# Kernel optimization log

Hardware: AMD Instinct MI355X
Metric: run time of the kernel (lower is better)

The kernel has to match this reference:

```python
import jax, jax.numpy as jnp
import numpy as np

RECON_W = 0.1
CONT_W = 0.2
EPS = 1e-7  # BCE log clamp (torch clamps log at -100; eps-clip is the jax analogue)


def setup_inputs() -> dict:
    key = jax.random.key(0)
    k1, k2, k3, k4 = jax.random.split(key, 4)
    B, M = 256, 4096
    predictions = jax.random.uniform(k1, (B, M, 9), dtype=jnp.float32)
    targets = jax.random.uniform(k2, (B, M, 9), dtype=jnp.float32)
    reconstructed = jax.random.normal(k3, (B, 1, 128, 128), dtype=jnp.float32)
    images = jax.random.normal(k4, (B, 1, 128, 128), dtype=jnp.float32)
    return {"predictions": predictions, "targets": targets,
            "reconstructed": reconstructed, "images": images}


def _continuity_loss(p3, valid_mask):
    # p3: [B, M, 2]; valid_mask: [B, M] bool
    # For each valid slot i, find the next valid slot j > i and accumulate
    # mean(|p3[i] - p3[j]|) -- vectorized replacement for the ragged double loop.
    B, M, _ = p3.shape
    idx = jnp.arange(M, dtype=jnp.int32)
    BIG = jnp.int32(M)
    pos = jnp.where(valid_mask, idx[None, :], BIG)              # [B, M]
    # suffix min over j >= i of pos, then shift to get strict j > i
    suf = jnp.flip(jax.lax.cummin(jnp.flip(pos, axis=1), axis=1), axis=1)
    nxt = jnp.concatenate([suf[:, 1:], jnp.full((B, 1), BIG, jnp.int32)], axis=1)
    pair_valid = valid_mask & (nxt < BIG)                       # [B, M]
    nxt_c = jnp.clip(nxt, 0, M - 1)
    p3_next = jnp.take_along_axis(p3, nxt_c[..., None], axis=1)  # [B, M, 2]
    dist = jnp.abs(p3 - p3_next).mean(axis=-1)                  # [B, M]
    return jnp.sum(dist * pair_valid.astype(p3.dtype)) / B


def _loss(predictions, targets, reconstructed, images):
    target_curves = targets[..., :8]
    target_validity = targets[..., 8:9]
    valid_mask = target_validity[..., 0] > 0.5                  # [B, M]
    fmask = valid_mask.astype(predictions.dtype)
    n_valid = jnp.sum(fmask)

    def masked_l1(pred, tgt, width):
        num = jnp.sum(jnp.abs(pred - tgt) * fmask[..., None])
        return jnp.where(n_valid > 0, num / jnp.maximum(n_valid * width, 1.0), 0.0)

    coord_loss = masked_l1(predictions[..., :6], target_curves[..., :6], 6.0)
    width_loss = masked_l1(predictions[..., 6:8], target_curves[..., 6:8], 2.0)

    p = jnp.clip(predictions[..., 8:9], EPS, 1.0 - EPS)
    t = target_validity
    validity_loss = jnp.mean(-(t * jnp.log(p) + (1.0 - t) * jnp.log(1.0 - p)))

    continuity_loss = _continuity_loss(predictions[..., 4:6], valid_mask)
    reconstruction_loss = jnp.mean((reconstructed - images) ** 2)

    total = (coord_loss + width_loss + 2.0 * validity_loss
             + CONT_W * continuity_loss + RECON_W * reconstruction_loss)
    return total


def reference(predictions, targets, reconstructed, images):
    return _loss(predictions, targets, reconstructed, images)
```

## Files before the change

### kernel.cpp

```cpp
#include <hip/hip_runtime.h>
#include <math.h>

#define B_DIM 256
#define M_DIM 4096
#define EPSV 1e-7f


__global__ __launch_bounds__(1024) void main_loss_kernel(
    const float* __restrict__ pred, const float* __restrict__ tgt,
    double* __restrict__ ws)
{
    __shared__ float s_p4[M_DIM];
    __shared__ float s_p5[M_DIM];
    __shared__ unsigned long long s_words[M_DIM / 64];
    __shared__ float s_red[16][5];

    const int b    = blockIdx.x;
    const int t    = threadIdx.x;
    const int lane = t & 63;
    const int wave = t >> 6;

    const float* prow = pred + (size_t)b * M_DIM * 9;
    const float* trow = tgt  + (size_t)b * M_DIM * 9;

    float coord_s = 0.f, width_s = 0.f, val_s = 0.f, nval_s = 0.f;
    bool valid_k[4];

    #pragma unroll
    for (int k = 0; k < 4; ++k) {
        const int m = k * 1024 + t;
        const float* p = prow + m * 9;
        const float* q = trow + m * 9;
        float p0 = p[0], p1 = p[1], p2 = p[2], p3 = p[3], p4 = p[4],
              p5 = p[5], p6 = p[6], p7 = p[7], p8 = p[8];
        float t0 = q[0], t1 = q[1], t2 = q[2], t3 = q[3], t4 = q[4],
              t5 = q[5], t6 = q[6], t7 = q[7], t8 = q[8];

        bool valid = (t8 > 0.5f);
        float fm = valid ? 1.f : 0.f;
        coord_s += fm * (fabsf(p0 - t0) + fabsf(p1 - t1) + fabsf(p2 - t2) +
                         fabsf(p3 - t3) + fabsf(p4 - t4) + fabsf(p5 - t5));
        width_s += fm * (fabsf(p6 - t6) + fabsf(p7 - t7));
        nval_s  += fm;

        float pc = fminf(fmaxf(p8, EPSV), 1.0f - EPSV);
        val_s += -(t8 * logf(pc) + (1.0f - t8) * logf(1.0f - pc));

        s_p4[m] = p4;
        s_p5[m] = p5;
        valid_k[k] = valid;

        unsigned long long bal = __ballot(valid);
        if (lane == 0) s_words[k * 16 + wave] = bal;
    }
    __syncthreads();

    float cont_s = 0.f;
    #pragma unroll
    for (int k = 0; k < 4; ++k) {
        if (!valid_k[k]) continue;
        const int m   = k * 1024 + t;
        const int w   = m >> 6;
        const int bit = m & 63;
        unsigned long long mask = s_words[w];
        mask &= (bit == 63) ? 0ULL : (~0ULL << (bit + 1));
        int nxt = -1;
        if (mask) {
            nxt = (w << 6) + __builtin_ctzll(mask);
        } else {
            for (int w2 = w + 1; w2 < (M_DIM / 64); ++w2) {
                unsigned long long mw = s_words[w2];
                if (mw) { nxt = (w2 << 6) + __builtin_ctzll(mw); break; }
            }
        }
        if (nxt >= 0) {
            cont_s += 0.5f * (fabsf(s_p4[m] - s_p4[nxt]) +
                              fabsf(s_p5[m] - s_p5[nxt]));
        }
    }

    float vals[5] = {coord_s, width_s, val_s, nval_s, cont_s};
    #pragma unroll
    for (int i = 0; i < 5; ++i) {
        float v = vals[i];
        #pragma unroll
        for (int off = 32; off > 0; off >>= 1) v += __shfl_down(v, off, 64);
        vals[i] = v;
    }
    if (lane == 0) {
        #pragma unroll
        for (int i = 0; i < 5; ++i) s_red[wave][i] = vals[i];
    }
    __syncthreads();
    if (t == 0) {
        float acc[5] = {0.f, 0.f, 0.f, 0.f, 0.f};
        for (int wv = 0; wv < 16; ++wv)
            #pragma unroll
            for (int i = 0; i < 5; ++i) acc[i] += s_red[wv][i];
        atomicAdd(&ws[0], (double)acc[0]);
        atomicAdd(&ws[1], (double)acc[1]);
        atomicAdd(&ws[2], (double)acc[2]);
        atomicAdd(&ws[3], (double)acc[3]);
        atomicAdd(&ws[4], (double)acc[4]);
    }
}

__global__ __launch_bounds__(256) void recon_kernel(
    const float4* __restrict__ rec, const float4* __restrict__ img,
    double* __restrict__ ws, int n4)
{
    int idx    = blockIdx.x * blockDim.x + threadIdx.x;
    int stride = gridDim.x * blockDim.x;
    float s = 0.f;
    for (int i = idx; i < n4; i += stride) {
        float4 r  = rec[i];
        float4 im = img[i];
        float d0 = r.x - im.x, d1 = r.y - im.y, d2 = r.z - im.z, d3 = r.w - im.w;
        s += d0 * d0 + d1 * d1 + d2 * d2 + d3 * d3;
    }
    #pragma unroll
    for (int off = 32; off > 0; off >>= 1) s += __shfl_down(s, off, 64);
    __shared__ float sred[4];
    int lane = threadIdx.x & 63, wave = threadIdx.x >> 6;
    if (lane == 0) sred[wave] = s;
    __syncthreads();
    if (threadIdx.x == 0) {
        float a = sred[0] + sred[1] + sred[2] + sred[3];
        atomicAdd(&ws[5], (double)a);
    }
}

__global__ void finalize_kernel(const double* __restrict__ ws,
                                float* __restrict__ out)
{
    double coord_num = ws[0];
    double width_num = ws[1];
    double val_sum   = ws[2];
    double nv        = ws[3];
    double cont      = ws[4];
    double recon     = ws[5];

    double coord = (nv > 0.0) ? coord_num / fmax(nv * 6.0, 1.0) : 0.0;
    double width = (nv > 0.0) ? width_num / fmax(nv * 2.0, 1.0) : 0.0;
    double validity = val_sum / ((double)B_DIM * (double)M_DIM);
    double contl    = cont / (double)B_DIM;
    double reconl   = recon / ((double)B_DIM * 128.0 * 128.0);

    out[0] = (float)(coord + width + 2.0 * validity + 0.2 * contl + 0.1 * reconl);
}

extern "C" void kernel_launch(void* const* d_in, const int* in_sizes, int n_in,
                              void* d_out, int out_size, void* d_ws, size_t ws_size,
                              hipStream_t stream) {
    const float* pred = (const float*)d_in[0];
    const float* tgt  = (const float*)d_in[1];
    const float* rec  = (const float*)d_in[2];
    const float* img  = (const float*)d_in[3];
    double* ws = (double*)d_ws;

    hipMemsetAsync(d_ws, 0, 6 * sizeof(double), stream);

    main_loss_kernel<<<B_DIM, 1024, 0, stream>>>(pred, tgt, ws);

    const int n4 = (B_DIM * 128 * 128) / 4;
    recon_kernel<<<1024, 256, 0, stream>>>((const float4*)rec, (const float4*)img, ws, n4);

    finalize_kernel<<<1, 1, 0, stream>>>(ws, (float*)d_out);
}
```

Baseline: 156.2 us.

## Fuse loss, reconstruction and finalize into one kernel with coalesced float4 loads

Merges the main loss, reconstruction MSE and finalize kernels into a single launch. Extra blocks handle the MSE, and a last-block-done atomic counter computes the final scalar. The main path now reads prediction and target rows as coalesced float4 vectors instead of stride-9 scalar loads, taking validity bits from a ballot bitmask built in an earlier pass over column 8. It also switches to fast __logf. The cost is an extra strided read of column 8 and a per-element bitmask lookup, plus slightly lower log precision.

```diff
diff --git a/kernel.cpp b/kernel.cpp
--- a/kernel.cpp
+++ b/kernel.cpp
@@ -4,149 +4,170 @@
 #define B_DIM 256
 #define M_DIM 4096
 #define EPSV 1e-7f
+#define ROW_FLOATS (M_DIM * 9)
+#define ROW_F4     (ROW_FLOATS / 4)
+#define THREADS    1024
+#define RECON_BLOCKS 256
+#define GRID (B_DIM + RECON_BLOCKS)
 
 
-__global__ __launch_bounds__(1024) void main_loss_kernel(
+__global__ __launch_bounds__(1024) void fused_loss_kernel(
     const float* __restrict__ pred, const float* __restrict__ tgt,
-    double* __restrict__ ws)
+    const float4* __restrict__ rec, const float4* __restrict__ img,
+    double* __restrict__ ws, float* __restrict__ out)
 {
     __shared__ float s_p4[M_DIM];
     __shared__ float s_p5[M_DIM];
     __shared__ unsigned long long s_words[M_DIM / 64];
     __shared__ float s_red[16][5];
 
-    const int b    = blockIdx.x;
     const int t    = threadIdx.x;
     const int lane = t & 63;
     const int wave = t >> 6;
 
-    const float* prow = pred + (size_t)b * M_DIM * 9;
-    const float* trow = tgt  + (size_t)b * M_DIM * 9;
+    if (blockIdx.x >= B_DIM) {
+        const int n4     = (B_DIM * 128 * 128) / 4;
+        const int stride = RECON_BLOCKS * THREADS;
+        int idx = (blockIdx.x - B_DIM) * THREADS + t;
+        float s = 0.f;
+        #pragma unroll
+        for (int i = 0; i < 4; ++i) {
+            float4 r = rec[idx]; float4 m = img[idx];
+            float d0 = r.x - m.x, d1 = r.y - m.y, d2 = r.z - m.z, d3 = r.w - m.w;
+            s += d0 * d0 + d1 * d1 + d2 * d2 + d3 * d3;
+            idx += stride;
+        }
+        #pragma unroll
+        for (int off = 32; off > 0; off >>= 1) s += __shfl_down(s, off, 64);
+        if (lane == 0) s_red[wave][0] = s;
+        __syncthreads();
+        if (t == 0) {
+            float a = 0.f;
+            for (int w = 0; w < 16; ++w) a += s_red[w][0];
+            atomicAdd(&ws[5], (double)a);
+        }
+    } else {
+        const int b = blockIdx.x;
+        const float* prow = pred + (size_t)b * ROW_FLOATS;
+        const float* trow = tgt  + (size_t)b * ROW_FLOATS;
 
-    float coord_s = 0.f, width_s = 0.f, val_s = 0.f, nval_s = 0.f;
-    bool valid_k[4];
+        float val_s = 0.f, nval_s = 0.f;
+        bool valid_k[4];
+        #pragma unroll
+        for (int k = 0; k < 4; ++k) {
+            const int m = k * 1024 + t;
+            float t8 = trow[m * 9 + 8];
+            float p8 = prow[m * 9 + 8];
+            bool valid = (t8 > 0.5f);
+            valid_k[k] = valid;
+            nval_s += valid ? 1.f : 0.f;
+            float pc = fminf(fmaxf(p8, EPSV), 1.0f - EPSV);
+            val_s += -(t8 * __logf(pc) + (1.0f - t8) * __logf(1.0f - pc));
+            unsigned long long bal = __ballot(valid);
+            if (lane == 0) s_words[k * 16 + wave] = bal;
+        }
+        __syncthreads();
 
-    #pragma unroll
-    for (int k = 0; k < 4; ++k) {
-        const int m = k * 1024 + t;
-        const float* p = prow + m * 9;
-        const float* q = trow + m * 9;
-        float p0 = p[0], p1 = p[1], p2 = p[2], p3 = p[3], p4 = p[4],
-              p5 = p[5], p6 = p[6], p7 = p[7], p8 = p[8];
-        float t0 = q[0], t1 = q[1], t2 = q[2], t3 = q[3], t4 = q[4],
-              t5 = q[5], t6 = q[6], t7 = q[7], t8 = q[8];
-
-        bool valid = (t8 > 0.5f);
-        float fm = valid ? 1.f : 0.f;
-        coord_s += fm * (fabsf(p0 - t0) + fabsf(p1 - t1) + fabsf(p2 - t2) +
-                         fabsf(p3 - t3) + fabsf(p4 - t4) + fabsf(p5 - t5));
-        width_s += fm * (fabsf(p6 - t6) + fabsf(p7 - t7));
-        nval_s  += fm;
-
-        float pc = fminf(fmaxf(p8, EPSV), 1.0f - EPSV);
-        val_s += -(t8 * logf(pc) + (1.0f - t8) * logf(1.0f - pc));
-
-        s_p4[m] = p4;
-        s_p5[m] = p5;
-        valid_k[k] = valid;
-
-        unsigned long long bal = __ballot(valid);
-        if (lane == 0) s_words[k * 16 + wave] = bal;
-    }
-    __syncthreads();
-
-    float cont_s = 0.f;
-    #pragma unroll
-    for (int k = 0; k < 4; ++k) {
-        if (!valid_k[k]) continue;
-        const int m   = k * 1024 + t;
-        const int w   = m >> 6;
-        const int bit = m & 63;
-        unsigned long long mask = s_words[w];
-        mask &= (bit == 63) ? 0ULL : (~0ULL << (bit + 1));
-        int nxt = -1;
-        if (mask) {
-            nxt = (w << 6) + __builtin_ctzll(mask);
-        } else {
-            for (int w2 = w + 1; w2 < (M_DIM / 64); ++w2) {
-                unsigned long long mw = s_words[w2];
-                if (mw) { nxt = (w2 << 6) + __builtin_ctzll(mw); break; }
+        float coord_s = 0.f, width_s = 0.f;
+        const float4* pf4 = (const float4*)prow;
+        const float4* tf4 = (const float4*)trow;
+        #pragma unroll
+        for (int i = 0; i < ROW_F4 / THREADS; ++i) {
+            int f = i * THREADS + t;
+            float4 pv = pf4[f];
+            float4 tv = tf4[f];
+            int j0 = f * 4;
+            int m  = j0 / 9;
+            int c  = j0 - m * 9;
+            float pe[4] = {pv.x, pv.y, pv.z, pv.w};
+            float te[4] = {tv.x, tv.y, tv.z, tv.w};
+            #pragma unroll
+            for (int k = 0; k < 4; ++k) {
+                float fm = (float)((s_words[m >> 6] >> (m & 63)) & 1ULL);
+                float ad = fabsf(pe[k] - te[k]);
+                if (c < 6)      coord_s += fm * ad;
+                else if (c < 8) width_s += fm * ad;
+                if (c == 4)      s_p4[m] = pe[k];
+                else if (c == 5) s_p5[m] = pe[k];
+                ++c; if (c == 9) { c = 0; ++m; }
             }
         }
-        if (nxt >= 0) {
-            cont_s += 0.5f * (fabsf(s_p4[m] - s_p4[nxt]) +
-                              fabsf(s_p5[m] - s_p5[nxt]));
+        __syncthreads();
+
+        float cont_s = 0.f;
+        #pragma unroll
+        for (int k = 0; k < 4; ++k) {
+            if (!valid_k[k]) continue;
+            const int m   = k * 1024 + t;
+            const int w   = m >> 6;
+            const int bit = m & 63;
+            unsigned long long mask = s_words[w];
+            mask &= (bit == 63) ? 0ULL : (~0ULL << (bit + 1));
+            int nxt = -1;
+            if (mask) {
+                nxt = (w << 6) + __builtin_ctzll(mask);
+            } else {
+                for (int w2 = w + 1; w2 < (M_DIM / 64); ++w2) {
+                    unsigned long long mw = s_words[w2];
+                    if (mw) { nxt = (w2 << 6) + __builtin_ctzll(mw); break; }
+                }
+            }
+            if (nxt >= 0) {
+                cont_s += 0.5f * (fabsf(s_p4[m] - s_p4[nxt]) +
+                                  fabsf(s_p5[m] - s_p5[nxt]));
+            }
+        }
+
+        float vals[5] = {coord_s, width_s, val_s, nval_s, cont_s};
+        #pragma unroll
+        for (int i = 0; i < 5; ++i) {
+            float v = vals[i];
+            #pragma unroll
+            for (int off = 32; off > 0; off >>= 1) v += __shfl_down(v, off, 64);
+            vals[i] = v;
+        }
+        if (lane == 0) {
+            #pragma unroll
+            for (int i = 0; i < 5; ++i) s_red[wave][i] = vals[i];
+        }
+        __syncthreads();
+        if (t == 0) {
+            float acc[5] = {0.f, 0.f, 0.f, 0.f, 0.f};
+            for (int wv = 0; wv < 16; ++wv)
+                #pragma unroll
+                for (int i = 0; i < 5; ++i) acc[i] += s_red[wv][i];
+            atomicAdd(&ws[0], (double)acc[0]);
+            atomicAdd(&ws[1], (double)acc[1]);
+            atomicAdd(&ws[2], (double)acc[2]);
+            atomicAdd(&ws[3], (double)acc[3]);
+            atomicAdd(&ws[4], (double)acc[4]);
         }
     }
 
-    float vals[5] = {coord_s, width_s, val_s, nval_s, cont_s};
-    #pragma unroll
-    for (int i = 0; i < 5; ++i) {
-        float v = vals[i];
-        #pragma unroll
-        for (int off = 32; off > 0; off >>= 1) v += __shfl_down(v, off, 64);
-        vals[i] = v;
-    }
-    if (lane == 0) {
-        #pragma unroll
-        for (int i = 0; i < 5; ++i) s_red[wave][i] = vals[i];
-    }
     __syncthreads();
     if (t == 0) {
-        float acc[5] = {0.f, 0.f, 0.f, 0.f, 0.f};
-        for (int wv = 0; wv < 16; ++wv)
-            #pragma unroll
-            for (int i = 0; i < 5; ++i) acc[i] += s_red[wv][i];
-        atomicAdd(&ws[0], (double)acc[0]);
-        atomicAdd(&ws[1], (double)acc[1]);
-        atomicAdd(&ws[2], (double)acc[2]);
-        atomicAdd(&ws[3], (double)acc[3]);
-        atomicAdd(&ws[4], (double)acc[4]);
+        __threadfence();
+        unsigned long long* cnt = (unsigned long long*)&ws[6];
+        unsigned long long old = atomicAdd(cnt, 1ULL);
+        if (old == (unsigned long long)(GRID - 1)) {
+            __threadfence();
+            double coord_num = atomicAdd(&ws[0], 0.0);
+            double width_num = atomicAdd(&ws[1], 0.0);
+            double val_sum   = atomicAdd(&ws[2], 0.0);
+            double nv        = atomicAdd(&ws[3], 0.0);
+            double cont      = atomicAdd(&ws[4], 0.0);
+            double recon     = atomicAdd(&ws[5], 0.0);
+
+            double coord = (nv > 0.0) ? coord_num / fmax(nv * 6.0, 1.0) : 0.0;
+            double width = (nv > 0.0) ? width_num / fmax(nv * 2.0, 1.0) : 0.0;
+            double validity = val_sum / ((double)B_DIM * (double)M_DIM);
+            double contl    = cont / (double)B_DIM;
+            double reconl   = recon / ((double)B_DIM * 128.0 * 128.0);
+
+            out[0] = (float)(coord + width + 2.0 * validity +
+                             0.2 * contl + 0.1 * reconl);
+        }
     }
-}
-
-__global__ __launch_bounds__(256) void recon_kernel(
-    const float4* __restrict__ rec, const float4* __restrict__ img,
-    double* __restrict__ ws, int n4)
-{
-    int idx    = blockIdx.x * blockDim.x + threadIdx.x;
-    int stride = gridDim.x * blockDim.x;
-    float s = 0.f;
-    for (int i = idx; i < n4; i += stride) {
-        float4 r  = rec[i];
-        float4 im = img[i];
-        float d0 = r.x - im.x, d1 = r.y - im.y, d2 = r.z - im.z, d3 = r.w - im.w;
-        s += d0 * d0 + d1 * d1 + d2 * d2 + d3 * d3;
-    }
-    #pragma unroll
-    for (int off = 32; off > 0; off >>= 1) s += __shfl_down(s, off, 64);
-    __shared__ float sred[4];
-    int lane = threadIdx.x & 63, wave = threadIdx.x >> 6;
-    if (lane == 0) sred[wave] = s;
-    __syncthreads();
-    if (threadIdx.x == 0) {
-        float a = sred[0] + sred[1] + sred[2] + sred[3];
-        atomicAdd(&ws[5], (double)a);
-    }
-}
-
-__global__ void finalize_kernel(const double* __restrict__ ws,
-                                float* __restrict__ out)
-{
-    double coord_num = ws[0];
-    double width_num = ws[1];
-    double val_sum   = ws[2];
-    double nv        = ws[3];
-    double cont      = ws[4];
-    double recon     = ws[5];
-
-    double coord = (nv > 0.0) ? coord_num / fmax(nv * 6.0, 1.0) : 0.0;
-    double width = (nv > 0.0) ? width_num / fmax(nv * 2.0, 1.0) : 0.0;
-    double validity = val_sum / ((double)B_DIM * (double)M_DIM);
-    double contl    = cont / (double)B_DIM;
-    double reconl   = recon / ((double)B_DIM * 128.0 * 128.0);
-
-    out[0] = (float)(coord + width + 2.0 * validity + 0.2 * contl + 0.1 * reconl);
 }
 
 extern "C" void kernel_launch(void* const* d_in, const int* in_sizes, int n_in,
@@ -158,12 +179,8 @@
     const float* img  = (const float*)d_in[3];
     double* ws = (double*)d_ws;
 
-    hipMemsetAsync(d_ws, 0, 6 * sizeof(double), stream);
+    hipMemsetAsync(d_ws, 0, 7 * sizeof(double), stream);
 
-    main_loss_kernel<<<B_DIM, 1024, 0, stream>>>(pred, tgt, ws);
-
-    const int n4 = (B_DIM * 128 * 128) / 4;
-    recon_kernel<<<1024, 256, 0, stream>>>((const float4*)rec, (const float4*)img, ws, n4);
-
-    finalize_kernel<<<1, 1, 0, stream>>>(ws, (float*)d_out);
+    fused_loss_kernel<<<GRID, THREADS, 0, stream>>>(
+        pred, tgt, (const float4*)rec, (const float4*)img, ws, (float*)d_out);
 }
```

Result: slower. 203.1 us (+30.1%).

## Split each row into quarter blocks and stitch continuity pairs in finalize

Applied to the files above, without the earlier changes.

The main loss kernel now runs four 256-thread blocks per row instead of one 1024-thread block. Each block records its first and last valid slot's coordinates in a small workspace, and the finalize kernel adds the continuity terms that cross block boundaries. The intent is more, smaller blocks for better occupancy and load balance. The change also uses fast __logf for the BCE term and doubles the recon kernel grid, which adds boundary-stitching logic and slight precision differences.

```diff
diff --git a/kernel.cpp b/kernel.cpp
--- a/kernel.cpp
+++ b/kernel.cpp
@@ -4,39 +4,46 @@
 #define B_DIM 256
 #define M_DIM 4096
 #define EPSV 1e-7f
-
-
-__global__ __launch_bounds__(1024) void main_loss_kernel(
+#define QPR   4
+#define QSIZE (M_DIM / QPR)
+#define K1_THREADS 256
+#define K1_ELEMS   (QSIZE / K1_THREADS)
+
+
+__global__ __launch_bounds__(K1_THREADS, 4) void row_loss_kernel(
     const float* __restrict__ pred, const float* __restrict__ tgt,
-    double* __restrict__ ws)
+    double* __restrict__ ws, float* __restrict__ rec_ws)
 {
-    __shared__ float s_p4[M_DIM];
-    __shared__ float s_p5[M_DIM];
-    __shared__ unsigned long long s_words[M_DIM / 64];
-    __shared__ float s_red[16][5];
-
-    const int b    = blockIdx.x;
+    __shared__ float s_p4[QSIZE];
+    __shared__ float s_p5[QSIZE];
+    __shared__ unsigned long long s_words[QSIZE / 64];
+    __shared__ float s_red[4][5];
+
+    const int q    = blockIdx.x;
+    const int row  = q >> 2;
+    const int qi   = q & 3;
     const int t    = threadIdx.x;
     const int lane = t & 63;
     const int wave = t >> 6;
 
-    const float* prow = pred + (size_t)b * M_DIM * 9;
-    const float* trow = tgt  + (size_t)b * M_DIM * 9;
+    const float* prow = pred + ((size_t)row * M_DIM + qi * QSIZE) * 9;
+    const float* trow = tgt  + ((size_t)row * M_DIM + qi * QSIZE) * 9;
 
     float coord_s = 0.f, width_s = 0.f, val_s = 0.f, nval_s = 0.f;
-    bool valid_k[4];
-
-    #pragma unroll
-    for (int k = 0; k < 4; ++k) {
-        const int m = k * 1024 + t;
+    bool valid_k[K1_ELEMS];
+
+    #pragma unroll
+    for (int k = 0; k < K1_ELEMS; ++k) {
+        const int m = k * K1_THREADS + t;
         const float* p = prow + m * 9;
-        const float* q = trow + m * 9;
+        const float* qq = trow + m * 9;
         float p0 = p[0], p1 = p[1], p2 = p[2], p3 = p[3], p4 = p[4],
               p5 = p[5], p6 = p[6], p7 = p[7], p8 = p[8];
-        float t0 = q[0], t1 = q[1], t2 = q[2], t3 = q[3], t4 = q[4],
-              t5 = q[5], t6 = q[6], t7 = q[7], t8 = q[8];
+        float t0 = qq[0], t1 = qq[1], t2 = qq[2], t3 = qq[3], t4 = qq[4],
+              t5 = qq[5], t6 = qq[6], t7 = qq[7], t8 = qq[8];
 
         bool valid = (t8 > 0.5f);
+        valid_k[k] = valid;
         float fm = valid ? 1.f : 0.f;
         coord_s += fm * (fabsf(p0 - t0) + fabsf(p1 - t1) + fabsf(p2 - t2) +
                          fabsf(p3 - t3) + fabsf(p4 - t4) + fabsf(p5 - t5));
@@ -44,22 +51,20 @@
         nval_s  += fm;
 
         float pc = fminf(fmaxf(p8, EPSV), 1.0f - EPSV);
-        val_s += -(t8 * logf(pc) + (1.0f - t8) * logf(1.0f - pc));
+        val_s += -(t8 * __logf(pc) + (1.0f - t8) * __logf(1.0f - pc));
 
         s_p4[m] = p4;
         s_p5[m] = p5;
-        valid_k[k] = valid;
-
         unsigned long long bal = __ballot(valid);
-        if (lane == 0) s_words[k * 16 + wave] = bal;
+        if (lane == 0) s_words[k * 4 + wave] = bal;
     }
     __syncthreads();
 
     float cont_s = 0.f;
     #pragma unroll
-    for (int k = 0; k < 4; ++k) {
+    for (int k = 0; k < K1_ELEMS; ++k) {
         if (!valid_k[k]) continue;
-        const int m   = k * 1024 + t;
+        const int m   = k * K1_THREADS + t;
         const int w   = m >> 6;
         const int bit = m & 63;
         unsigned long long mask = s_words[w];
@@ -68,7 +73,7 @@
         if (mask) {
             nxt = (w << 6) + __builtin_ctzll(mask);
         } else {
-            for (int w2 = w + 1; w2 < (M_DIM / 64); ++w2) {
+            for (int w2 = w + 1; w2 < (QSIZE / 64); ++w2) {
                 unsigned long long mw = s_words[w2];
                 if (mw) { nxt = (w2 << 6) + __builtin_ctzll(mw); break; }
             }
@@ -94,7 +99,7 @@
     __syncthreads();
     if (t == 0) {
         float acc[5] = {0.f, 0.f, 0.f, 0.f, 0.f};
-        for (int wv = 0; wv < 16; ++wv)
+        for (int wv = 0; wv < 4; ++wv)
             #pragma unroll
             for (int i = 0; i < 5; ++i) acc[i] += s_red[wv][i];
         atomicAdd(&ws[0], (double)acc[0]);
@@ -102,20 +107,39 @@
         atomicAdd(&ws[2], (double)acc[2]);
         atomicAdd(&ws[3], (double)acc[3]);
         atomicAdd(&ws[4], (double)acc[4]);
+
+        int first = -1, last = -1;
+        for (int w = 0; w < (QSIZE / 64); ++w) {
+            unsigned long long mw = s_words[w];
+            if (mw) { first = (w << 6) + __builtin_ctzll(mw); break; }
+        }
+        for (int w = (QSIZE / 64) - 1; w >= 0; --w) {
+            unsigned long long mw = s_words[w];
+            if (mw) { last = (w << 6) + 63 - __builtin_clzll(mw); break; }
+        }
+        float* r = rec_ws + q * 6;
+        if (first >= 0) {
+            r[0] = 1.f;
+            r[1] = s_p4[first]; r[2] = s_p5[first];
+            r[3] = s_p4[last];  r[4] = s_p5[last];
+        } else {
+            r[0] = 0.f; r[1] = 0.f; r[2] = 0.f; r[3] = 0.f; r[4] = 0.f;
+        }
+        r[5] = 0.f;
     }
 }
 
 __global__ __launch_bounds__(256) void recon_kernel(
     const float4* __restrict__ rec, const float4* __restrict__ img,
-    double* __restrict__ ws, int n4)
+    double* __restrict__ ws)
 {
-    int idx    = blockIdx.x * blockDim.x + threadIdx.x;
-    int stride = gridDim.x * blockDim.x;
+    const int n4     = (B_DIM * 128 * 128) / 4;
+    const int stride = gridDim.x * blockDim.x;
+    int idx = blockIdx.x * blockDim.x + threadIdx.x;
     float s = 0.f;
     for (int i = idx; i < n4; i += stride) {
-        float4 r  = rec[i];
-        float4 im = img[i];
-        float d0 = r.x - im.x, d1 = r.y - im.y, d2 = r.z - im.z, d3 = r.w - im.w;
+        float4 r = rec[i]; float4 m = img[i];
+        float d0 = r.x - m.x, d1 = r.y - m.y, d2 = r.z - m.z, d3 = r.w - m.w;
         s += d0 * d0 + d1 * d1 + d2 * d2 + d3 * d3;
     }
     #pragma unroll
@@ -125,28 +149,55 @@
     if (lane == 0) sred[wave] = s;
     __syncthreads();
     if (threadIdx.x == 0) {
-        float a = sred[0] + sred[1] + sred[2] + sred[3];
-        atomicAdd(&ws[5], (double)a);
-    }
-}
-
-__global__ void finalize_kernel(const double* __restrict__ ws,
-                                float* __restrict__ out)
+        atomicAdd(&ws[5], (double)(sred[0] + sred[1] + sred[2] + sred[3]));
+    }
+}
+
+__global__ __launch_bounds__(256) void finalize_kernel(
+    const double* __restrict__ ws, const float* __restrict__ rec_ws,
+    float* __restrict__ out)
 {
-    double coord_num = ws[0];
-    double width_num = ws[1];
-    double val_sum   = ws[2];
-    double nv        = ws[3];
-    double cont      = ws[4];
-    double recon     = ws[5];
-
-    double coord = (nv > 0.0) ? coord_num / fmax(nv * 6.0, 1.0) : 0.0;
-    double width = (nv > 0.0) ? width_num / fmax(nv * 2.0, 1.0) : 0.0;
-    double validity = val_sum / ((double)B_DIM * (double)M_DIM);
-    double contl    = cont / (double)B_DIM;
-    double reconl   = recon / ((double)B_DIM * 128.0 * 128.0);
-
-    out[0] = (float)(coord + width + 2.0 * validity + 0.2 * contl + 0.1 * reconl);
+    const int t = threadIdx.x;
+    float cont_extra = 0.f;
+    {
+        const float* base = rec_ws + t * QPR * 6;
+        bool  have = false;
+        float pl4 = 0.f, pl5 = 0.f;
+        #pragma unroll
+        for (int q = 0; q < QPR; ++q) {
+            const float* r = base + q * 6;
+            if (r[0] > 0.5f) {
+                if (have)
+                    cont_extra += 0.5f * (fabsf(pl4 - r[1]) + fabsf(pl5 - r[2]));
+                pl4 = r[3]; pl5 = r[4];
+                have = true;
+            }
+        }
+    }
+    #pragma unroll
+    for (int off = 32; off > 0; off >>= 1)
+        cont_extra += __shfl_down(cont_extra, off, 64);
+    __shared__ float sred[4];
+    int lane = t & 63, wave = t >> 6;
+    if (lane == 0) sred[wave] = cont_extra;
+    __syncthreads();
+    if (t == 0) {
+        double cont = ws[4] + (double)(sred[0] + sred[1] + sred[2] + sred[3]);
+        double coord_num = ws[0];
+        double width_num = ws[1];
+        double val_sum   = ws[2];
+        double nv        = ws[3];
+        double recon     = ws[5];
+
+        double coord = (nv > 0.0) ? coord_num / fmax(nv * 6.0, 1.0) : 0.0;
+        double width = (nv > 0.0) ? width_num / fmax(nv * 2.0, 1.0) : 0.0;
+        double validity = val_sum / ((double)B_DIM * (double)M_DIM);
+        double contl    = cont / (double)B_DIM;
+        double reconl   = recon / ((double)B_DIM * 128.0 * 128.0);
+
+        out[0] = (float)(coord + width + 2.0 * validity +
+                         0.2 * contl + 0.1 * reconl);
+    }
 }
 
 extern "C" void kernel_launch(void* const* d_in, const int* in_sizes, int n_in,
@@ -157,13 +208,11 @@
     const float* rec  = (const float*)d_in[2];
     const float* img  = (const float*)d_in[3];
     double* ws = (double*)d_ws;
+    float* rec_ws = (float*)((char*)d_ws + 64);
 
     hipMemsetAsync(d_ws, 0, 6 * sizeof(double), stream);
 
-    main_loss_kernel<<<B_DIM, 1024, 0, stream>>>(pred, tgt, ws);
-
-    const int n4 = (B_DIM * 128 * 128) / 4;
-    recon_kernel<<<1024, 256, 0, stream>>>((const float4*)rec, (const float4*)img, ws, n4);
-
-    finalize_kernel<<<1, 1, 0, stream>>>(ws, (float*)d_out);
-}
+    row_loss_kernel<<<B_DIM * QPR, K1_THREADS, 0, stream>>>(pred, tgt, ws, rec_ws);
+    recon_kernel<<<2048, 256, 0, stream>>>((const float4*)rec, (const float4*)img, ws);
+    finalize_kernel<<<1, 256, 0, stream>>>(ws, rec_ws, (float*)d_out);
+}
```

New measurement: 208.3 us. 33.4% more time.

## Vectorize row loads as float4 with contiguous per-thread elements and interleaved ballot bits

Applied to the files above, without the earlier changes.

Each thread now owns four consecutive elements of a row and loads them as nine float4 vectors per input, in place of strided scalar loads at a 36-byte stride. Because the element-to-thread mapping changed, the validity ballots are re-interleaved with a bit-spread routine so the shared bitmask stays in element order. The p4/p5 values go to shared memory as float4 stores. The change also switches to fast __logf, asks for 4 blocks per CU in launch bounds, and doubles the recon grid, at the cost of higher register pressure from holding 72 floats per thread.

```diff
diff --git a/kernel.cpp b/kernel.cpp
--- a/kernel.cpp
+++ b/kernel.cpp
@@ -4,9 +4,23 @@
 #define B_DIM 256
 #define M_DIM 4096
 #define EPSV 1e-7f
+#define THREADS 1024
 
 
-__global__ __launch_bounds__(1024) void main_loss_kernel(
+__device__ __forceinline__ unsigned long long spread4(unsigned long long x) {
+    x &= 0xFFFFULL;
+    x = (x | (x << 24)) & 0x000000FF000000FFULL;
+    x = (x | (x << 12)) & 0x000F000F000F000FULL;
+    x = (x | (x << 6))  & 0x0303030303030303ULL;
+    x = (x | (x << 3))  & 0x1111111111111111ULL;
+    return x;
+}
+
+#define VF(arr, i) (((i) & 3) == 0 ? arr[(i) >> 2].x : \
+                    ((i) & 3) == 1 ? arr[(i) >> 2].y : \
+                    ((i) & 3) == 2 ? arr[(i) >> 2].z : arr[(i) >> 2].w)
+
+__global__ __launch_bounds__(THREADS, 4) void row_loss_kernel(
     const float* __restrict__ pred, const float* __restrict__ tgt,
     double* __restrict__ ws)
 {
@@ -20,23 +34,30 @@
     const int lane = t & 63;
     const int wave = t >> 6;
 
-    const float* prow = pred + (size_t)b * M_DIM * 9;
-    const float* trow = tgt  + (size_t)b * M_DIM * 9;
+    const float4* pf4 = (const float4*)(pred + (size_t)b * M_DIM * 9);
+    const float4* tf4 = (const float4*)(tgt  + (size_t)b * M_DIM * 9);
+
+    float4 pr[9], tr[9];
+    #pragma unroll
+    for (int j = 0; j < 9; ++j) pr[j] = pf4[9 * t + j];
+    #pragma unroll
+    for (int j = 0; j < 9; ++j) tr[j] = tf4[9 * t + j];
 
     float coord_s = 0.f, width_s = 0.f, val_s = 0.f, nval_s = 0.f;
-    bool valid_k[4];
+    float vp4[4], vp5[4];
+    bool vld[4];
 
     #pragma unroll
-    for (int k = 0; k < 4; ++k) {
-        const int m = k * 1024 + t;
-        const float* p = prow + m * 9;
-        const float* q = trow + m * 9;
-        float p0 = p[0], p1 = p[1], p2 = p[2], p3 = p[3], p4 = p[4],
-              p5 = p[5], p6 = p[6], p7 = p[7], p8 = p[8];
-        float t0 = q[0], t1 = q[1], t2 = q[2], t3 = q[3], t4 = q[4],
-              t5 = q[5], t6 = q[6], t7 = q[7], t8 = q[8];
+    for (int e = 0; e < 4; ++e) {
+        float p0 = VF(pr, e * 9 + 0), p1 = VF(pr, e * 9 + 1), p2 = VF(pr, e * 9 + 2);
+        float p3 = VF(pr, e * 9 + 3), p4 = VF(pr, e * 9 + 4), p5 = VF(pr, e * 9 + 5);
+        float p6 = VF(pr, e * 9 + 6), p7 = VF(pr, e * 9 + 7), p8 = VF(pr, e * 9 + 8);
+        float t0 = VF(tr, e * 9 + 0), t1 = VF(tr, e * 9 + 1), t2 = VF(tr, e * 9 + 2);
+        float t3 = VF(tr, e * 9 + 3), t4 = VF(tr, e * 9 + 4), t5 = VF(tr, e * 9 + 5);
+        float t6 = VF(tr, e * 9 + 6), t7 = VF(tr, e * 9 + 7), t8 = VF(tr, e * 9 + 8);
 
         bool valid = (t8 > 0.5f);
+        vld[e] = valid;
         float fm = valid ? 1.f : 0.f;
         coord_s += fm * (fabsf(p0 - t0) + fabsf(p1 - t1) + fabsf(p2 - t2) +
                          fabsf(p3 - t3) + fabsf(p4 - t4) + fabsf(p5 - t5));
@@ -44,22 +65,32 @@
         nval_s  += fm;
 
         float pc = fminf(fmaxf(p8, EPSV), 1.0f - EPSV);
-        val_s += -(t8 * logf(pc) + (1.0f - t8) * logf(1.0f - pc));
+        val_s += -(t8 * __logf(pc) + (1.0f - t8) * __logf(1.0f - pc));
 
-        s_p4[m] = p4;
-        s_p5[m] = p5;
-        valid_k[k] = valid;
+        vp4[e] = p4;
+        vp5[e] = p5;
+    }
 
-        unsigned long long bal = __ballot(valid);
-        if (lane == 0) s_words[k * 16 + wave] = bal;
+    ((float4*)s_p4)[t] = make_float4(vp4[0], vp4[1], vp4[2], vp4[3]);
+    ((float4*)s_p5)[t] = make_float4(vp5[0], vp5[1], vp5[2], vp5[3]);
+
+    unsigned long long bal[4];
+    #pragma unroll
+    for (int e = 0; e < 4; ++e) bal[e] = __ballot(vld[e]);
+    if (lane < 4) {
+        unsigned long long w = 0;
+        #pragma unroll
+        for (int j = 0; j < 4; ++j)
+            w |= spread4(bal[j] >> (16 * lane)) << j;
+        s_words[wave * 4 + lane] = w;
     }
     __syncthreads();
 
     float cont_s = 0.f;
     #pragma unroll
-    for (int k = 0; k < 4; ++k) {
-        if (!valid_k[k]) continue;
-        const int m   = k * 1024 + t;
+    for (int e = 0; e < 4; ++e) {
+        if (!vld[e]) continue;
+        const int m   = 4 * t + e;
         const int w   = m >> 6;
         const int bit = m & 63;
         unsigned long long mask = s_words[w];
@@ -107,15 +138,15 @@
 
 __global__ __launch_bounds__(256) void recon_kernel(
     const float4* __restrict__ rec, const float4* __restrict__ img,
-    double* __restrict__ ws, int n4)
+    double* __restrict__ ws)
 {
-    int idx    = blockIdx.x * blockDim.x + threadIdx.x;
-    int stride = gridDim.x * blockDim.x;
+    const int n4     = (B_DIM * 128 * 128) / 4;
+    const int stride = gridDim.x * blockDim.x;
+    int idx = blockIdx.x * blockDim.x + threadIdx.x;
     float s = 0.f;
     for (int i = idx; i < n4; i += stride) {
-        float4 r  = rec[i];
-        float4 im = img[i];
-        float d0 = r.x - im.x, d1 = r.y - im.y, d2 = r.z - im.z, d3 = r.w - im.w;
+        float4 r = rec[i]; float4 m = img[i];
+        float d0 = r.x - m.x, d1 = r.y - m.y, d2 = r.z - m.z, d3 = r.w - m.w;
         s += d0 * d0 + d1 * d1 + d2 * d2 + d3 * d3;
     }
     #pragma unroll
@@ -125,8 +156,7 @@
     if (lane == 0) sred[wave] = s;
     __syncthreads();
     if (threadIdx.x == 0) {
-        float a = sred[0] + sred[1] + sred[2] + sred[3];
-        atomicAdd(&ws[5], (double)a);
+        atomicAdd(&ws[5], (double)(sred[0] + sred[1] + sred[2] + sred[3]));
     }
 }
 
@@ -146,7 +176,8 @@
     double contl    = cont / (double)B_DIM;
     double reconl   = recon / ((double)B_DIM * 128.0 * 128.0);
 
-    out[0] = (float)(coord + width + 2.0 * validity + 0.2 * contl + 0.1 * reconl);
+    out[0] = (float)(coord + width + 2.0 * validity +
+                     0.2 * contl + 0.1 * reconl);
 }
 
 extern "C" void kernel_launch(void* const* d_in, const int* in_sizes, int n_in,
@@ -160,10 +191,7 @@
 
     hipMemsetAsync(d_ws, 0, 6 * sizeof(double), stream);
 
-    main_loss_kernel<<<B_DIM, 1024, 0, stream>>>(pred, tgt, ws);
-
-    const int n4 = (B_DIM * 128 * 128) / 4;
-    recon_kernel<<<1024, 256, 0, stream>>>((const float4*)rec, (const float4*)img, ws, n4);
-
+    row_loss_kernel<<<B_DIM, THREADS, 0, stream>>>(pred, tgt, ws);
+    recon_kernel<<<2048, 256, 0, stream>>>((const float4*)rec, (const float4*)img, ws);
     finalize_kernel<<<1, 1, 0, stream>>>(ws, (float*)d_out);
 }
```

After: 169.8 us. 8.7% more time.
